# Kernel tuning notes

Hardware: AMD Instinct MI355X
Metric: run time of the kernel (lower is better)

## Reference

```python
import jax, jax.numpy as jnp
import numpy as np

B, T, DIM, H = 2, 2048, 1024, 16
HD = DIM // H


def setup_inputs() -> dict:
    key = jax.random.key(0)
    k1, k2, k3 = jax.random.split(key, 3)
    std = 1.0 / np.sqrt(DIM)
    x = jax.random.normal(k1, (B, T, DIM), dtype=jnp.float32)
    # torch Linear(dim, 3*dim).weight is [3*dim, dim]; we store the transposed
    # [dim, 3*dim] layout so forward is x @ W_qkv (same math).
    W_qkv = jax.random.uniform(k2, (DIM, 3 * DIM), dtype=jnp.float32, minval=-std, maxval=std)
    W_proj = jax.random.uniform(k3, (DIM, DIM), dtype=jnp.float32, minval=-std, maxval=std)
    return {"x": x, "W_qkv": W_qkv, "W_proj": W_proj}


def reference(x, W_qkv, W_proj):
    Bv, Tv, C = x.shape
    # qkv projection -> [B, T, 3, H, HD] -> q,k,v each [B, H, T, HD]
    qkv = (x @ W_qkv).reshape(Bv, Tv, 3, H, HD)
    qkv = jnp.transpose(qkv, (2, 0, 3, 1, 4))
    q, k, v = qkv[0], qkv[1], qkv[2]
    scale = jnp.asarray(np.sqrt(HD), dtype=x.dtype)
    scores = jnp.einsum('bhqd,bhkd->bhqk', q, k) / scale
    causal = jnp.tril(jnp.ones((Tv, Tv), dtype=bool))  # [T, T]
    scores = jnp.where(causal[None, None, :, :], scores, -jnp.inf)
    attn = jax.nn.softmax(scores, axis=-1)  # [B, H, T, T]
    # entropy per query position, averaged over heads -> [B, T]
    entropy = -(attn * jnp.log(attn + 1e-9)).sum(axis=-1).mean(axis=1)
    # dropout is identity in eval mode
    out = jnp.einsum('bhqk,bhkd->bhqd', attn, v)
    out = jnp.transpose(out, (0, 2, 1, 3)).reshape(Bv, Tv, C)
    return out @ W_proj, entropy
```

## Files before the change

### kernel.cpp

```cpp
#include <hip/hip_runtime.h>


typedef unsigned short u16;
typedef __attribute__((ext_vector_type(8))) __bf16 bf16x8;
typedef __attribute__((ext_vector_type(4))) float float4v;

#define BQ 2
#define TQ 2048
#define DIMQ 1024
#define HQ 16
#define HDQ 64

__device__ __forceinline__ float4v mfma16(bf16x8 a, bf16x8 b, float4v c) {
    return __builtin_amdgcn_mfma_f32_16x16x32_bf16(a, b, c, 0, 0, 0);
}

__device__ __forceinline__ u16 f2bf(float f) {
    unsigned x = __float_as_uint(f);
    return (u16)((x + 0x7FFFu + ((x >> 16) & 1u)) >> 16);
}

__device__ __forceinline__ uint4 cvt8(float4 a, float4 b) {
    union { uint4 v; u16 u[8]; } r;
    r.u[0] = f2bf(a.x); r.u[1] = f2bf(a.y); r.u[2] = f2bf(a.z); r.u[3] = f2bf(a.w);
    r.u[4] = f2bf(b.x); r.u[5] = f2bf(b.y); r.u[6] = f2bf(b.z); r.u[7] = f2bf(b.w);
    return r.v;
}

__device__ __forceinline__ void async16(const u16* g, u16* l) {
    __builtin_amdgcn_global_load_lds(
        (const __attribute__((address_space(1))) void*)g,
        (__attribute__((address_space(3))) void*)l, 16, 0, 0);
}

__global__ __launch_bounds__(256) void cvt_bf16(
    const float* __restrict__ in, u16* __restrict__ out, int n)
{
    int i = (blockIdx.x * 256 + threadIdx.x) * 8;
    if (i < n) {
        float4 a = *(const float4*)(in + i);
        float4 b = *(const float4*)(in + i + 4);
        *(uint4*)(out + i) = cvt8(a, b);
    }
}

__global__ __launch_bounds__(256) void tr_cvt(
    const float* __restrict__ in, u16* __restrict__ out, int R, int C)
{
    __shared__ float T[64][68];
    const int t = threadIdx.x;
    const int k0 = blockIdx.y * 64, n0 = blockIdx.x * 64;
    {
        int r = t >> 2, cc = (t & 3) << 4;
        const float* src = in + (size_t)(k0 + r) * C + n0 + cc;
        float4 v0 = ((const float4*)src)[0];
        float4 v1 = ((const float4*)src)[1];
        float4 v2 = ((const float4*)src)[2];
        float4 v3 = ((const float4*)src)[3];
        *(float4*)&T[r][cc + 0]  = v0;
        *(float4*)&T[r][cc + 4]  = v1;
        *(float4*)&T[r][cc + 8]  = v2;
        *(float4*)&T[r][cc + 12] = v3;
    }
    __syncthreads();
    {
        int nr = t >> 2, kc = (t & 3) << 4;
        union { uint4 v; u16 u[8]; } o0, o1;
#pragma unroll
        for (int j = 0; j < 8; ++j) o0.u[j] = f2bf(T[kc + j][nr]);
#pragma unroll
        for (int j = 0; j < 8; ++j) o1.u[j] = f2bf(T[kc + 8 + j][nr]);
        u16* dst = out + (size_t)(n0 + nr) * R + k0 + kc;
        ((uint4*)dst)[0] = o0.v;
        *(uint4*)(dst + 8) = o1.v;
    }
}

template <int TILEM, int MODE>
__global__ __launch_bounds__(256) void gemm128(
    const u16* __restrict__ A, const u16* __restrict__ Bt,
    int M, int N, int K,
    u16* __restrict__ Qo, u16* __restrict__ Ko, u16* __restrict__ Vt,
    float* __restrict__ Of)
{
    constexpr int MT = TILEM / 32;
    __shared__ u16 As[TILEM * 64];
    __shared__ u16 Bs[128 * 64];

    const int tid = threadIdx.x;
    const int bm = blockIdx.y, bn = blockIdx.x;
    const int wave = tid >> 6, lane = tid & 63;
    const int quad = lane >> 4, c = lane & 15;
    const int wm = wave >> 1, wn = wave & 1;
    const int x7 = c & 7;

    const float4v z = {0.f, 0.f, 0.f, 0.f};
    float4v acc[MT][4];
#pragma unroll
    for (int mt = 0; mt < MT; ++mt)
#pragma unroll
        for (int tn = 0; tn < 4; ++tn) acc[mt][tn] = z;

    const int srow = tid >> 3;
    const int schunk8 = (((tid & 7) ^ (srow & 7)) << 3);
    const u16* ga = A  + (size_t)(bm * TILEM + srow) * K + schunk8;
    const u16* gb = Bt + (size_t)(bn * 128  + srow) * K + schunk8;

    for (int kc = 0; kc < K; kc += 64) {
#pragma unroll
        for (int p = 0; p < MT; ++p)
            async16(ga + kc + (size_t)(p * 32) * K, As + p * 2048 + tid * 8);
#pragma unroll
        for (int p = 0; p < 4; ++p)
            async16(gb + kc + (size_t)(p * 32) * K, Bs + p * 2048 + tid * 8);
        __syncthreads();

        bf16x8 af[MT][2], bfr[4][2];
#pragma unroll
        for (int mt = 0; mt < MT; ++mt) {
            int base = (wm * (TILEM / 2) + mt * 16 + c) * 64;
            af[mt][0] = *(const bf16x8*)&As[base + ((quad ^ x7) << 3)];
            af[mt][1] = *(const bf16x8*)&As[base + (((quad + 4) ^ x7) << 3)];
        }
#pragma unroll
        for (int tn = 0; tn < 4; ++tn) {
            int base = (wn * 64 + tn * 16 + c) * 64;
            bfr[tn][0] = *(const bf16x8*)&Bs[base + ((quad ^ x7) << 3)];
            bfr[tn][1] = *(const bf16x8*)&Bs[base + (((quad + 4) ^ x7) << 3)];
        }
#pragma unroll
        for (int kk = 0; kk < 2; ++kk)
#pragma unroll
            for (int mt = 0; mt < MT; ++mt)
#pragma unroll
                for (int tn = 0; tn < 4; ++tn)
                    acc[mt][tn] = mfma16(af[mt][kk], bfr[tn][kk], acc[mt][tn]);
        __syncthreads();
    }

#pragma unroll
    for (int mt = 0; mt < MT; ++mt)
#pragma unroll
        for (int tn = 0; tn < 4; ++tn) {
            int gm0 = bm * TILEM + wm * (TILEM / 2) + mt * 16 + quad * 4;
            int gn  = bn * 128 + wn * 64 + tn * 16 + c;
            if (MODE == 0) {
                int s = gn >> 10, h = (gn >> 6) & 15, d = gn & 63;
                int b = gm0 >> 11, t0 = gm0 & 2047;
                size_t bh = (size_t)(b * HQ + h);
                if (s == 2) {
                    union { unsigned long long w; u16 u[4]; } pk;
#pragma unroll
                    for (int r = 0; r < 4; ++r) pk.u[r] = f2bf(acc[mt][tn][r]);
                    *(unsigned long long*)&Vt[(bh * HDQ + d) * TQ + t0] = pk.w;
                } else {
                    u16* dst = (s == 0) ? Qo : Ko;
                    float sc = (s == 0) ? 0.125f : 1.0f;
#pragma unroll
                    for (int r = 0; r < 4; ++r)
                        dst[(bh * TQ + t0 + r) * HDQ + d] = f2bf(acc[mt][tn][r] * sc);
                }
            } else {
#pragma unroll
                for (int r = 0; r < 4; ++r)
                    Of[(size_t)(gm0 + r) * N + gn] = acc[mt][tn][r];
            }
        }
}

__global__ __launch_bounds__(256) void attn_kernel(
    const u16* __restrict__ Q, const u16* __restrict__ K,
    const u16* __restrict__ Vt, u16* __restrict__ AO,
    float* __restrict__ Ent)
{
    const int qt1 = blockIdx.x;
    const int qt2 = 31 - qt1;
    const int bh = blockIdx.y;
    const int tid = threadIdx.x;
    const int wave = tid >> 6, lane = tid & 63;
    const int quad = lane >> 4, c = lane & 15;
    const int x7 = c & 7;

    __shared__ u16 Ks[2][64 * 64];
    __shared__ u16 Vs[2][64 * 64];
    __shared__ u16 Ps[4][16 * 64];

    const u16* Qp = Q  + (size_t)bh * TQ * HDQ;
    const u16* Kp = K  + (size_t)bh * TQ * HDQ;
    const u16* Vp = Vt + (size_t)bh * HDQ * TQ;

    const int q0[2] = { qt1 * 64 + wave * 16, qt2 * 64 + wave * 16 };

    bf16x8 qf[2][2];
#pragma unroll
    for (int s = 0; s < 2; ++s) {
        const u16* qr = Qp + (size_t)(q0[s] + c) * HDQ;
        qf[s][0] = *(const bf16x8*)(qr + quad * 8);
        qf[s][1] = *(const bf16x8*)(qr + 32 + quad * 8);
    }

    const float4v z = {0.f, 0.f, 0.f, 0.f};
    float4v oacc[2][4];
#pragma unroll
    for (int s = 0; s < 2; ++s)
#pragma unroll
        for (int tn = 0; tn < 4; ++tn) oacc[s][tn] = z;
    float lp[2][4] = {{0.f,0.f,0.f,0.f},{0.f,0.f,0.f,0.f}};
    float tp[2][4] = {{0.f,0.f,0.f,0.f},{0.f,0.f,0.f,0.f}};
    const float MX = 12.0f;

    u16* psw = &Ps[wave][0];
    const int ntile = qt2 + 1;

    const int srow = tid >> 3;
    const int schunk8 = (((tid & 7) ^ (srow & 7)) << 3);
    const u16* ka = Kp + (size_t)srow * HDQ + schunk8;
    const u16* va = Vp + (size_t)srow * TQ + schunk8;

    {
        async16(ka, Ks[0] + tid * 8);
        async16(ka + (size_t)32 * HDQ, Ks[0] + 2048 + tid * 8);
        async16(va, Vs[0] + tid * 8);
        async16(va + (size_t)32 * TQ, Vs[0] + 2048 + tid * 8);
    }

    for (int jt = 0; jt < ntile; ++jt) {
        __syncthreads();
        if (jt + 1 < ntile) {
            int nb = (jt + 1) & 1;
            async16(ka + (size_t)((jt + 1) * 64) * HDQ, Ks[nb] + tid * 8);
            async16(ka + (size_t)((jt + 1) * 64 + 32) * HDQ, Ks[nb] + 2048 + tid * 8);
            async16(va + (jt + 1) * 64, Vs[nb] + tid * 8);
            async16(va + (size_t)32 * TQ + (jt + 1) * 64, Vs[nb] + 2048 + tid * 8);
        }
        const u16* ksb = Ks[jt & 1];
        const u16* vsb = Vs[jt & 1];

        bf16x8 kf[4][2], vf[4][2];
#pragma unroll
        for (int tn = 0; tn < 4; ++tn) {
            int base = (tn * 16 + c) * 64;
            kf[tn][0] = *(const bf16x8*)&ksb[base + ((quad ^ x7) << 3)];
            kf[tn][1] = *(const bf16x8*)&ksb[base + (((quad + 4) ^ x7) << 3)];
            vf[tn][0] = *(const bf16x8*)&vsb[base + ((quad ^ x7) << 3)];
            vf[tn][1] = *(const bf16x8*)&vsb[base + (((quad + 4) ^ x7) << 3)];
        }

#pragma unroll
        for (int s = 0; s < 2; ++s) {
            if (s == 0 && jt > qt1) continue;
            float4v sacc[4] = {z, z, z, z};
#pragma unroll
            for (int tn = 0; tn < 4; ++tn) {
                sacc[tn] = mfma16(qf[s][0], kf[tn][0], sacc[tn]);
                sacc[tn] = mfma16(qf[s][1], kf[tn][1], sacc[tn]);
            }
            const int diag = (s == 0) ? qt1 : qt2;
            if (jt == diag) {
#pragma unroll
                for (int tn = 0; tn < 4; ++tn)
#pragma unroll
                    for (int r = 0; r < 4; ++r) {
                        int kg = jt * 64 + tn * 16 + c;
                        int qg = q0[s] + quad * 4 + r;
                        if (kg > qg) sacc[tn][r] = -1e30f;
                    }
            }
#pragma unroll
            for (int tn = 0; tn < 4; ++tn)
#pragma unroll
                for (int r = 0; r < 4; ++r) {
                    float sv = sacc[tn][r];
                    float p = __expf(sv - MX);
                    lp[s][r] += p;
                    tp[s][r] += p * sv;
                    int row = quad * 4 + r;
                    int chunk = tn * 2 + (c >> 3);
                    psw[row * 64 + ((chunk ^ (row & 7)) << 3) + x7] =
                        (u16)(__float_as_uint(p) >> 16);
                }
            int prow = c * 64;
            bf16x8 pf0 = *(const bf16x8*)&psw[prow + ((quad ^ x7) << 3)];
            bf16x8 pf1 = *(const bf16x8*)&psw[prow + (((quad + 4) ^ x7) << 3)];
#pragma unroll
            for (int tn = 0; tn < 4; ++tn) {
                oacc[s][tn] = mfma16(pf0, vf[tn][0], oacc[s][tn]);
                oacc[s][tn] = mfma16(pf1, vf[tn][1], oacc[s][tn]);
            }
        }
    }

#pragma unroll
    for (int s = 0; s < 2; ++s)
#pragma unroll
        for (int r = 0; r < 4; ++r) {
#pragma unroll
            for (int off = 1; off < 16; off <<= 1) {
                lp[s][r] += __shfl_xor(lp[s][r], off);
                tp[s][r] += __shfl_xor(tp[s][r], off);
            }
        }

    const int b = bh >> 4, h = bh & 15;
#pragma unroll
    for (int s = 0; s < 2; ++s) {
#pragma unroll
        for (int tn = 0; tn < 4; ++tn)
#pragma unroll
            for (int r = 0; r < 4; ++r) {
                int qg = q0[s] + quad * 4 + r;
                int d = tn * 16 + c;
                AO[((size_t)(b * TQ + qg)) * DIMQ + h * HDQ + d] =
                    f2bf(oacc[s][tn][r] / lp[s][r]);
            }
        if (c == 0) {
#pragma unroll
            for (int r = 0; r < 4; ++r) {
                int qg = q0[s] + quad * 4 + r;
                Ent[(size_t)bh * TQ + qg] =
                    MX + logf(lp[s][r]) - tp[s][r] / lp[s][r];
            }
        }
    }
}

__global__ __launch_bounds__(256) void ent_avg_kernel(
    const float* __restrict__ Ent, float* __restrict__ out)
{
    int i = blockIdx.x * blockDim.x + threadIdx.x;
    int b = i >> 11, t = i & 2047;
    float s = 0.f;
#pragma unroll
    for (int h = 0; h < HQ; ++h) s += Ent[((size_t)(b * HQ + h)) * TQ + t];
    out[i] = s * (1.0f / HQ);
}

extern "C" void kernel_launch(void* const* d_in, const int* in_sizes, int n_in,
                              void* d_out, int out_size, void* d_ws, size_t ws_size,
                              hipStream_t stream) {
    const float* x     = (const float*)d_in[0];
    const float* Wqkv  = (const float*)d_in[1];
    const float* Wproj = (const float*)d_in[2];
    float* out = (float*)d_out;

    const size_t NE = (size_t)BQ * HQ * TQ * HDQ;
    u16* Qb   = (u16*)d_ws;
    u16* Kb   = Qb + NE;
    u16* Vtb  = Kb + NE;
    u16* xb   = Vtb + NE;
    u16* Wt   = xb + NE;
    float* Ent = (float*)(Wt + (size_t)DIMQ * 3 * DIMQ);
    u16* AO = xb;
    u16* Wpt = Wt;

    cvt_bf16<<<dim3(2048), 256, 0, stream>>>(x, xb, BQ * TQ * DIMQ);
    tr_cvt<<<dim3(48, 16), 256, 0, stream>>>(Wqkv, Wt, DIMQ, 3 * DIMQ);
    gemm128<128, 0><<<dim3(24, 32), 256, 0, stream>>>(
        xb, Wt, BQ * TQ, 3 * DIMQ, DIMQ, Qb, Kb, Vtb, nullptr);
    tr_cvt<<<dim3(16, 16), 256, 0, stream>>>(Wproj, Wpt, DIMQ, DIMQ);
    attn_kernel<<<dim3(16, BQ * HQ), 256, 0, stream>>>(Qb, Kb, Vtb, AO, Ent);
    gemm128<64, 1><<<dim3(8, 64), 256, 0, stream>>>(
        AO, Wpt, BQ * TQ, DIMQ, DIMQ, nullptr, nullptr, nullptr, out);
    ent_avg_kernel<<<dim3(16), 256, 0, stream>>>(Ent, out + (size_t)BQ * TQ * DIMQ);
}
```

Before: 197.0 us.

## Double-buffer GEMM K loop, fuse prep conversions and entropy averaging into fewer launches

Switches the GEMM mainloop from single-buffered K=64 stages with two barriers per iteration to double-buffered K=32 stages, so the next tile's async loads overlap the current MFMAs with a single barrier per step. The x conversion and both weight transposes are merged into one prep kernel when the workspace is large enough. The entropy head-average is folded into the output-projection GEMM tail, removing two launches. Halving the K step doubles the number of barriers and iterations, and the smaller XOR swizzle may raise LDS bank conflicts.

```diff
diff --git a/kernel.cpp b/kernel.cpp
--- a/kernel.cpp
+++ b/kernel.cpp
@@ -33,25 +33,13 @@
         (__attribute__((address_space(3))) void*)l, 16, 0, 0);
 }
 
-__global__ __launch_bounds__(256) void cvt_bf16(
-    const float* __restrict__ in, u16* __restrict__ out, int n)
-{
-    int i = (blockIdx.x * 256 + threadIdx.x) * 8;
-    if (i < n) {
-        float4 a = *(const float4*)(in + i);
-        float4 b = *(const float4*)(in + i + 4);
-        *(uint4*)(out + i) = cvt8(a, b);
-    }
-}
-
-__global__ __launch_bounds__(256) void tr_cvt(
-    const float* __restrict__ in, u16* __restrict__ out, int R, int C)
-{
-    __shared__ float T[64][68];
-    const int t = threadIdx.x;
-    const int k0 = blockIdx.y * 64, n0 = blockIdx.x * 64;
+__device__ __forceinline__ void tr_tile(
+    const float* __restrict__ in, u16* __restrict__ out, int R, int C,
+    int tx, int ty, int tid, float (*T)[68])
+{
+    const int k0 = ty * 64, n0 = tx * 64;
     {
-        int r = t >> 2, cc = (t & 3) << 4;
+        int r = tid >> 2, cc = (tid & 3) << 4;
         const float* src = in + (size_t)(k0 + r) * C + n0 + cc;
         float4 v0 = ((const float4*)src)[0];
         float4 v1 = ((const float4*)src)[1];
@@ -64,7 +52,7 @@
     }
     __syncthreads();
     {
-        int nr = t >> 2, kc = (t & 3) << 4;
+        int nr = tid >> 2, kc = (tid & 3) << 4;
         union { uint4 v; u16 u[8]; } o0, o1;
 #pragma unroll
         for (int j = 0; j < 8; ++j) o0.u[j] = f2bf(T[kc + j][nr]);
@@ -76,23 +64,52 @@
     }
 }
 
+__global__ __launch_bounds__(256) void prep_kernel(
+    const float* __restrict__ x, const float* __restrict__ Wq,
+    const float* __restrict__ Wp,
+    u16* __restrict__ xb, u16* __restrict__ Wt, u16* __restrict__ Wpt)
+{
+    __shared__ float T[64][68];
+    const int bx = blockIdx.x, tid = threadIdx.x;
+    if (bx < 2048) {
+        int i = (bx * 256 + tid) * 8;
+        float4 a = *(const float4*)(x + i);
+        float4 b = *(const float4*)(x + i + 4);
+        *(uint4*)(xb + i) = cvt8(a, b);
+    } else if (bx < 2816) {
+        int bb = bx - 2048;
+        tr_tile(Wq, Wt, DIMQ, 3 * DIMQ, bb % 48, bb / 48, tid, T);
+    } else {
+        int bb = bx - 2816;
+        tr_tile(Wp, Wpt, DIMQ, DIMQ, bb & 15, bb >> 4, tid, T);
+    }
+}
+
+__global__ __launch_bounds__(256) void tr_cvt(
+    const float* __restrict__ in, u16* __restrict__ out, int R, int C)
+{
+    __shared__ float T[64][68];
+    tr_tile(in, out, R, C, blockIdx.x, blockIdx.y, threadIdx.x, T);
+}
+
 template <int TILEM, int MODE>
-__global__ __launch_bounds__(256) void gemm128(
+__global__ __launch_bounds__(256) void gemm_db(
     const u16* __restrict__ A, const u16* __restrict__ Bt,
     int M, int N, int K,
     u16* __restrict__ Qo, u16* __restrict__ Ko, u16* __restrict__ Vt,
-    float* __restrict__ Of)
+    float* __restrict__ Of, const float* __restrict__ EntIn)
 {
     constexpr int MT = TILEM / 32;
-    __shared__ u16 As[TILEM * 64];
-    __shared__ u16 Bs[128 * 64];
+    constexpr int AR = TILEM / 64;
+    __shared__ u16 As[2][TILEM * 32];
+    __shared__ u16 Bs[2][128 * 32];
 
     const int tid = threadIdx.x;
     const int bm = blockIdx.y, bn = blockIdx.x;
     const int wave = tid >> 6, lane = tid & 63;
     const int quad = lane >> 4, c = lane & 15;
     const int wm = wave >> 1, wn = wave & 1;
-    const int x7 = c & 7;
+    const int x3 = c & 3;
 
     const float4v z = {0.f, 0.f, 0.f, 0.f};
     float4v acc[MT][4];
@@ -101,41 +118,48 @@
 #pragma unroll
         for (int tn = 0; tn < 4; ++tn) acc[mt][tn] = z;
 
-    const int srow = tid >> 3;
-    const int schunk8 = (((tid & 7) ^ (srow & 7)) << 3);
+    const int srow = tid >> 2;
+    const int schunk8 = (((tid & 3) ^ (srow & 3)) << 3);
     const u16* ga = A  + (size_t)(bm * TILEM + srow) * K + schunk8;
     const u16* gb = Bt + (size_t)(bn * 128  + srow) * K + schunk8;
 
-    for (int kc = 0; kc < K; kc += 64) {
-#pragma unroll
-        for (int p = 0; p < MT; ++p)
-            async16(ga + kc + (size_t)(p * 32) * K, As + p * 2048 + tid * 8);
-#pragma unroll
-        for (int p = 0; p < 4; ++p)
-            async16(gb + kc + (size_t)(p * 32) * K, Bs + p * 2048 + tid * 8);
+#pragma unroll
+    for (int p = 0; p < AR; ++p)
+        async16(ga + (size_t)(p * 64) * K, As[0] + p * 2048 + tid * 8);
+#pragma unroll
+    for (int p = 0; p < 2; ++p)
+        async16(gb + (size_t)(p * 64) * K, Bs[0] + p * 2048 + tid * 8);
+
+    const int niter = K >> 5;
+    for (int it = 0; it < niter; ++it) {
         __syncthreads();
-
-        bf16x8 af[MT][2], bfr[4][2];
-#pragma unroll
-        for (int mt = 0; mt < MT; ++mt) {
-            int base = (wm * (TILEM / 2) + mt * 16 + c) * 64;
-            af[mt][0] = *(const bf16x8*)&As[base + ((quad ^ x7) << 3)];
-            af[mt][1] = *(const bf16x8*)&As[base + (((quad + 4) ^ x7) << 3)];
-        }
-#pragma unroll
-        for (int tn = 0; tn < 4; ++tn) {
-            int base = (wn * 64 + tn * 16 + c) * 64;
-            bfr[tn][0] = *(const bf16x8*)&Bs[base + ((quad ^ x7) << 3)];
-            bfr[tn][1] = *(const bf16x8*)&Bs[base + (((quad + 4) ^ x7) << 3)];
-        }
-#pragma unroll
-        for (int kk = 0; kk < 2; ++kk)
-#pragma unroll
-            for (int mt = 0; mt < MT; ++mt)
-#pragma unroll
-                for (int tn = 0; tn < 4; ++tn)
-                    acc[mt][tn] = mfma16(af[mt][kk], bfr[tn][kk], acc[mt][tn]);
-        __syncthreads();
+        if (it + 1 < niter) {
+            const int nb = (it + 1) & 1;
+            const int kc = (it + 1) * 32;
+#pragma unroll
+            for (int p = 0; p < AR; ++p)
+                async16(ga + kc + (size_t)(p * 64) * K, As[nb] + p * 2048 + tid * 8);
+#pragma unroll
+            for (int p = 0; p < 2; ++p)
+                async16(gb + kc + (size_t)(p * 64) * K, Bs[nb] + p * 2048 + tid * 8);
+        }
+        const u16* as = As[it & 1];
+        const u16* bs = Bs[it & 1];
+
+        bf16x8 af[MT], bfr[4];
+#pragma unroll
+        for (int mt = 0; mt < MT; ++mt)
+            af[mt] = *(const bf16x8*)&as[(wm * (TILEM / 2) + mt * 16 + c) * 32 +
+                                         ((quad ^ x3) << 3)];
+#pragma unroll
+        for (int tn = 0; tn < 4; ++tn)
+            bfr[tn] = *(const bf16x8*)&bs[(wn * 64 + tn * 16 + c) * 32 +
+                                          ((quad ^ x3) << 3)];
+#pragma unroll
+        for (int mt = 0; mt < MT; ++mt)
+#pragma unroll
+            for (int tn = 0; tn < 4; ++tn)
+                acc[mt][tn] = mfma16(af[mt], bfr[tn], acc[mt][tn]);
     }
 
 #pragma unroll
@@ -166,6 +190,15 @@
                     Of[(size_t)(gm0 + r) * N + gn] = acc[mt][tn][r];
             }
         }
+
+    if (MODE == 1 && bn == 0 && bm < 16) {
+        int i = bm * 256 + tid;
+        int b = i >> 11, t = i & 2047;
+        float s = 0.f;
+#pragma unroll
+        for (int h = 0; h < HQ; ++h) s += EntIn[((size_t)(b * HQ + h)) * TQ + t];
+        Of[(size_t)BQ * TQ * DIMQ + i] = s * (1.0f / HQ);
+    }
 }
 
 __global__ __launch_bounds__(256) void attn_kernel(
@@ -324,17 +357,6 @@
     }
 }
 
-__global__ __launch_bounds__(256) void ent_avg_kernel(
-    const float* __restrict__ Ent, float* __restrict__ out)
-{
-    int i = blockIdx.x * blockDim.x + threadIdx.x;
-    int b = i >> 11, t = i & 2047;
-    float s = 0.f;
-#pragma unroll
-    for (int h = 0; h < HQ; ++h) s += Ent[((size_t)(b * HQ + h)) * TQ + t];
-    out[i] = s * (1.0f / HQ);
-}
-
 extern "C" void kernel_launch(void* const* d_in, const int* in_sizes, int n_in,
                               void* d_out, int out_size, void* d_ws, size_t ws_size,
                               hipStream_t stream) {
@@ -344,22 +366,27 @@
     float* out = (float*)d_out;
 
     const size_t NE = (size_t)BQ * HQ * TQ * HDQ;
-    u16* Qb   = (u16*)d_ws;
-    u16* Kb   = Qb + NE;
-    u16* Vtb  = Kb + NE;
-    u16* xb   = Vtb + NE;
-    u16* Wt   = xb + NE;
-    float* Ent = (float*)(Wt + (size_t)DIMQ * 3 * DIMQ);
-    u16* AO = xb;
-    u16* Wpt = Wt;
-
-    cvt_bf16<<<dim3(2048), 256, 0, stream>>>(x, xb, BQ * TQ * DIMQ);
-    tr_cvt<<<dim3(48, 16), 256, 0, stream>>>(Wqkv, Wt, DIMQ, 3 * DIMQ);
-    gemm128<128, 0><<<dim3(24, 32), 256, 0, stream>>>(
-        xb, Wt, BQ * TQ, 3 * DIMQ, DIMQ, Qb, Kb, Vtb, nullptr);
-    tr_cvt<<<dim3(16, 16), 256, 0, stream>>>(Wproj, Wpt, DIMQ, DIMQ);
+    const size_t WQN = (size_t)3 * DIMQ * DIMQ;
+    const size_t WPN = (size_t)DIMQ * DIMQ;
+    u16* Qb  = (u16*)d_ws;
+    u16* Kb  = Qb + NE;
+    u16* Vtb = Kb + NE;
+    u16* xb  = Vtb + NE;
+    u16* Wt  = xb + NE;
+    u16* AO  = xb;
+
+    const size_t need = (4 * NE + WQN + WPN) * 2 + (size_t)BQ * HQ * TQ * 4;
+    const bool room = ws_size >= need;
+    u16* Wpt = room ? (Wt + WQN) : Wt;
+    float* Ent = room ? (float*)(Wpt + WPN) : (float*)(Wt + WQN);
+
+    prep_kernel<<<dim3(room ? 3072 : 2816), 256, 0, stream>>>(
+        x, Wqkv, Wproj, xb, Wt, Wpt);
+    gemm_db<128, 0><<<dim3(24, 32), 256, 0, stream>>>(
+        xb, Wt, BQ * TQ, 3 * DIMQ, DIMQ, Qb, Kb, Vtb, nullptr, nullptr);
+    if (!room)
+        tr_cvt<<<dim3(16, 16), 256, 0, stream>>>(Wproj, Wpt, DIMQ, DIMQ);
     attn_kernel<<<dim3(16, BQ * HQ), 256, 0, stream>>>(Qb, Kb, Vtb, AO, Ent);
-    gemm128<64, 1><<<dim3(8, 64), 256, 0, stream>>>(
-        AO, Wpt, BQ * TQ, DIMQ, DIMQ, nullptr, nullptr, nullptr, out);
-    ent_avg_kernel<<<dim3(16), 256, 0, stream>>>(Ent, out + (size_t)BQ * TQ * DIMQ);
-}
+    gemm_db<64, 1><<<dim3(8, 64), 256, 0, stream>>>(
+        AO, Wpt, BQ * TQ, DIMQ, DIMQ, nullptr, nullptr, nullptr, out, Ent);
+}
```

After: 183.4 us. 1.07x faster.
